# Kernel tuning notes

Hardware: AMD Instinct MI355X
Metric: run time of the kernel (lower is better)

The kernel has to match this reference:

```python
import jax, jax.numpy as jnp
import numpy as np

NEG = -1e9  # stands in for -inf; sparsemax thresholding makes these entries exactly 0


def sparsemax(z):
    """Sparsemax along the last axis (Martins & Astudillo 2016)."""
    K = z.shape[-1]
    z_sorted = -jnp.sort(-z, axis=-1)                      # descending
    kk = jnp.arange(1, K + 1, dtype=z.dtype)
    z_cum = jnp.cumsum(z_sorted, axis=-1)
    support = 1.0 + kk * z_sorted > z_cum                  # [..., K] bool
    k_sup = jnp.sum(support, axis=-1, keepdims=True).astype(z.dtype)
    z_sum = jnp.sum(jnp.where(support, z_sorted, 0.0), axis=-1, keepdims=True)
    tau = (z_sum - 1.0) / k_sup
    return jnp.maximum(z - tau, 0.0)


def setup_inputs() -> dict:
    key = jax.random.key(0)
    ks = jax.random.split(key, 7)
    b, t, e, h = 8, 1024, 128, 8
    x = jax.random.normal(ks[0], (b, t, e), dtype=jnp.float32)
    mask = jax.random.randint(ks[1], (b, t, t), 0, 2, dtype=jnp.int32)
    w_q = jax.random.normal(ks[2], (e, h * e), dtype=jnp.float32) * 0.05
    w_k = jax.random.normal(ks[3], (e, h * e), dtype=jnp.float32) * 0.05
    w_v = jax.random.normal(ks[4], (e, h * e), dtype=jnp.float32) * 0.05
    w_s = jax.random.normal(ks[5], (h, e), dtype=jnp.float32) * 0.05
    b_s = jnp.zeros((h,), dtype=jnp.float32)
    return {"x": x, "mask": mask, "w_q": w_q, "w_k": w_k, "w_v": w_v,
            "w_s": w_s, "b_s": b_s}


def reference(x, mask, w_q, w_k, w_v, w_s, b_s):
    b, t, e = x.shape
    h = w_s.shape[0]
    scale = 1.0 / jnp.sqrt(jnp.asarray(e, x.dtype))  # temperature = emb_dim**0.5

    # projections: each head gets FULL emb_dim width (per original module)
    q = (x @ w_q).reshape(b, t, h, e).transpose(2, 0, 1, 3)  # [h,b,t,e]
    k = (x @ w_k).reshape(b, t, h, e).transpose(2, 0, 1, 3)
    v = (x @ w_v).reshape(b, t, h, e).transpose(2, 0, 1, 3)

    attn = jnp.einsum('hbqe,hbke->hbqk', q * scale, k)       # [h,b,t,t]

    m = mask.astype(bool)[None]                              # [1,b,t,t], broadcast over heads
    inf_mask = jnp.all(m, axis=-1, keepdims=True)            # rows fully masked
    attn = jnp.where(m, NEG, attn)
    attn = jnp.where(inf_mask, 0.0, attn)
    attn = sparsemax(attn)
    attn = jnp.where(inf_mask, 0.0, attn)                    # dropout is identity (p=0)

    out = jnp.einsum('hbqk,hbke->hbqe', attn, v)             # [h,b,t,e]
    out = out.transpose(1, 2, 0, 3)                          # [b,t,h,e]

    sel = jax.nn.softmax(jnp.mean(x, axis=1) @ w_s.T + b_s, axis=-1)  # [b,h]
    return jnp.einsum('bh,bthe->bte', sel, out)              # gated head mix
```

## Files before the change

kernel.cpp:

```cpp
#include <hip/hip_runtime.h>
#include <hip/hip_bf16.h>
#include <math.h>

#define SCALE 0.08838834764831845f

using short8  = __attribute__((ext_vector_type(8))) short;
using short4v = __attribute__((ext_vector_type(4))) short;
using us4     = __attribute__((ext_vector_type(4))) unsigned short;
using f32x4   = __attribute__((ext_vector_type(4))) float;
typedef unsigned long long u64;
typedef unsigned short ushort_t;

static __device__ __forceinline__ ushort_t bf16_of(float f) {
    __hip_bfloat16 h = __float2bfloat16(f);
    return *reinterpret_cast<ushort_t*>(&h);
}
static __device__ __forceinline__ float f_of_bf16(unsigned int u) {
    union { unsigned int i; float f; } v; v.i = u << 16; return v.f;
}

__global__ __launch_bounds__(256)
void prep_all(const float* __restrict__ x, ushort_t* __restrict__ xb,
              const float* __restrict__ wq, const float* __restrict__ wk,
              const float* __restrict__ wv, ushort_t* __restrict__ Wt,
              const int* __restrict__ mask, u64* __restrict__ mp) {
    __shared__ float tile[64][129];
    const int bx = blockIdx.x;
    const int tid = threadIdx.x;
    if (bx < 1024) {
        const int i = bx * 256 + tid;
        float4 v = reinterpret_cast<const float4*>(x)[i];
        short4v o;
        o.x = (short)bf16_of(v.x); o.y = (short)bf16_of(v.y);
        o.z = (short)bf16_of(v.z); o.w = (short)bf16_of(v.w);
        reinterpret_cast<short4v*>(xb)[i] = o;
    } else if (bx < 1072) {
        const int wb = bx - 1024;
        const int mat = wb >> 4;
        const int n0 = (wb & 15) * 64;
        const float* W = (mat == 0) ? wq : (mat == 1) ? wk : wv;
        for (int idx = tid; idx < 8192; idx += 256) {
            const int k = idx >> 6, c = idx & 63;
            tile[c][k] = W[(size_t)k * 1024 + n0 + c];
        }
        __syncthreads();
        for (int idx = tid; idx < 8192; idx += 256) {
            const int c = idx >> 7, k = idx & 127;
            Wt[(size_t)(mat * 1024 + n0 + c) * 128 + k] = bf16_of(tile[c][k]);
        }
    } else {
        const int mb = bx - 1072;
        const int row = mb * 4 + (tid >> 6);
        const int l = tid & 63;
        const int* m = mask + (size_t)row * 1024;
        #pragma unroll
        for (int c = 0; c < 16; ++c) {
            u64 bm = __ballot(m[c * 64 + l] != 0);
            if (l == 0) mp[(size_t)row * 16 + c] = bm;
        }
    }
}

__global__ __launch_bounds__(256)
void proj_gemm(const ushort_t* __restrict__ xb, const ushort_t* __restrict__ Wt,
               ushort_t* __restrict__ Q, ushort_t* __restrict__ K,
               ushort_t* __restrict__ V) {
    const int tid = threadIdx.x;
    const int w = tid >> 6, l = tid & 63;
    const int l15 = l & 15, lq = l >> 4;
    const int m0 = blockIdx.x * 64;
    const int nb = blockIdx.y;
    const int mat = nb >> 4;
    const int n0 = (nb & 15) * 64;
    const int b = m0 >> 10;

    short8 af[4][4];
    #pragma unroll
    for (int at = 0; at < 4; ++at) {
        const ushort_t* ar = xb + (size_t)(m0 + at * 16 + l15) * 128 + lq * 8;
        #pragma unroll
        for (int f = 0; f < 4; ++f)
            af[at][f] = *reinterpret_cast<const short8*>(ar + f * 32);
    }
    const int ng = n0 + w * 16 + l15;
    const ushort_t* br = Wt + (size_t)(mat * 1024 + ng) * 128 + lq * 8;
    short8 bf[4];
    #pragma unroll
    for (int f = 0; f < 4; ++f)
        bf[f] = *reinterpret_cast<const short8*>(br + f * 32);
    f32x4 acc[4];
    #pragma unroll
    for (int at = 0; at < 4; ++at) acc[at] = (f32x4){0.f, 0.f, 0.f, 0.f};
    #pragma unroll
    for (int at = 0; at < 4; ++at)
        #pragma unroll
        for (int f = 0; f < 4; ++f)
            acc[at] = __builtin_amdgcn_mfma_f32_16x16x32_bf16(af[at][f], bf[f], acc[at], 0, 0, 0);

    const int h = ng >> 7, e = ng & 127;
    ushort_t* O = (mat == 0) ? Q : (mat == 1) ? K : V;
    const float scl = (mat == 0) ? SCALE : 1.0f;
    const size_t obase = (size_t)(h * 8 + b) * 131072 + e;
    #pragma unroll
    for (int at = 0; at < 4; ++at)
        #pragma unroll
        for (int r = 0; r < 4; ++r) {
            const int t = (m0 & 1023) + at * 16 + lq * 4 + r;
            O[obase + (size_t)t * 128] = bf16_of(acc[at][r] * scl);
        }
}

__global__ __launch_bounds__(1024)
void sel_kernel(const float* __restrict__ x, const float* __restrict__ wsl,
                const float* __restrict__ bsl, float* __restrict__ sel) {
    __shared__ float part[8][128];
    __shared__ float xm[128];
    __shared__ float lg[8];
    const int b = blockIdx.x;
    const int tid = threadIdx.x;
    const int e = tid & 127, tc = tid >> 7;
    float s = 0.f;
    for (int t = 0; t < 128; ++t)
        s += x[((size_t)b * 1024 + tc * 128 + t) * 128 + e];
    part[tc][e] = s;
    __syncthreads();
    if (tid < 128) {
        float tot = 0.f;
        #pragma unroll
        for (int i = 0; i < 8; ++i) tot += part[i][tid];
        xm[tid] = tot * (1.0f / 1024.0f);
    }
    __syncthreads();
    if (tid < 8) {
        float d = 0.f;
        for (int e2 = 0; e2 < 128; ++e2) d += xm[e2] * wsl[tid * 128 + e2];
        lg[tid] = d + bsl[tid];
    }
    __syncthreads();
    if (tid == 0) {
        float mx = lg[0];
        for (int hh = 1; hh < 8; ++hh) mx = fmaxf(mx, lg[hh]);
        float se = 0.f; float ex[8];
        for (int hh = 0; hh < 8; ++hh) { ex[hh] = expf(lg[hh] - mx); se += ex[hh]; }
        for (int hh = 0; hh < 8; ++hh) sel[b * 8 + hh] = ex[hh] / se;
    }
}

__global__ __launch_bounds__(512, 2)
void attn_kernel(const ushort_t* __restrict__ Qb, const ushort_t* __restrict__ Kb,
                 const ushort_t* __restrict__ Vb, const u64* __restrict__ mp,
                 const float* __restrict__ sel, float* __restrict__ out) {
    __shared__ float S[16 * 1024];
    __shared__ int cnt[16];
    unsigned int* list = reinterpret_cast<unsigned int*>(S);

    const int tid = threadIdx.x;
    const int w = tid >> 6, l = tid & 63;
    const int l15 = l & 15, lq = l >> 4;
    const int hb = (int)blockIdx.x >> 6;
    const int qt = (int)blockIdx.x & 63;
    const int h = hb >> 3, b = hb & 7;
    const int t0 = qt * 16;
    const size_t base = (size_t)hb * 131072;

    if (tid < 16) cnt[tid] = 0;

    short8 qa[4];
    {
        const ushort_t* qrp = Qb + base + (size_t)(t0 + l15) * 128 + lq * 8;
        #pragma unroll
        for (int f = 0; f < 4; ++f)
            qa[f] = *reinterpret_cast<const short8*>(qrp + f * 32);
    }

    f32x4 sc[8];
    #pragma unroll
    for (int i = 0; i < 8; ++i) {
        const int kt = w * 8 + i;
        const ushort_t* krow = Kb + base + (size_t)(kt * 16 + l15) * 128 + lq * 8;
        f32x4 acc = {0.f, 0.f, 0.f, 0.f};
        #pragma unroll
        for (int f = 0; f < 4; ++f) {
            short8 kb = *reinterpret_cast<const short8*>(krow + f * 32);
            acc = __builtin_amdgcn_mfma_f32_16x16x32_bf16(qa[f], kb, acc, 0, 0, 0);
        }
        sc[i] = acc;
    }

    const int rowbase = b * 1024 + t0;
    #pragma unroll
    for (int r = 0; r < 4; ++r) {
        const int q = lq * 4 + r;
        const u64* mrow = mp + (size_t)(rowbase + q) * 16 + w * 2;
        const u64 m0 = mrow[0], m1 = mrow[1];
        #pragma unroll
        for (int i = 0; i < 8; ++i) {
            const u64 mword = (i < 4) ? m0 : m1;
            const int bit = (i & 3) * 16 + l15;
            if ((mword >> bit) & 1ULL) sc[i][r] = -1e30f;
        }
    }

    #pragma unroll
    for (int r = 0; r < 4; ++r) {
        const int q = lq * 4 + r;
        #pragma unroll
        for (int i = 0; i < 8; ++i) {
            const int c = (w * 8 + i) * 4 + (l15 >> 2);
            const int cp = c ^ ((c >> 3) & 7) ^ (q & 7);
            S[q * 1024 + cp * 4 + (l15 & 3)] = sc[i][r];
        }
    }
    __syncthreads();

    const int qrow = 2 * w + (l & 1);
    const int lh = l >> 1;
    float z[32];
    #pragma unroll
    for (int j = 0; j < 8; ++j) {
        const int c = lh + 32 * j;
        const int cp = c ^ ((c >> 3) & 7) ^ (qrow & 7);
        float4 v = *reinterpret_cast<const float4*>(&S[qrow * 1024 + cp * 4]);
        z[4 * j + 0] = v.x; z[4 * j + 1] = v.y;
        z[4 * j + 2] = v.z; z[4 * j + 3] = v.w;
    }
    __syncthreads();

    float s0 = 0.f, c0 = 0.f;
    #pragma unroll
    for (int k = 0; k < 32; ++k) {
        const float zz = z[k];
        if (zz > -1e29f) { s0 += zz; c0 += 1.f; }
    }
    #pragma unroll
    for (int mm = 2; mm < 64; mm <<= 1) {
        s0 += __shfl_xor(s0, mm);
        c0 += __shfl_xor(c0, mm);
    }
    float tau = (c0 > 0.f) ? (s0 - 1.f) / c0 : 3e38f;
    float prev = c0;
    for (int it = 0; it < 64; ++it) {
        float s2 = 0.f, c2 = 0.f;
        #pragma unroll
        for (int k = 0; k < 32; ++k) {
            const float zz = z[k];
            if (zz > tau) { s2 += zz; c2 += 1.f; }
        }
        #pragma unroll
        for (int mm = 2; mm < 64; mm <<= 1) {
            s2 += __shfl_xor(s2, mm);
            c2 += __shfl_xor(c2, mm);
        }
        const int stable = (c2 == prev) ? 1 : 0;
        if (__all(stable)) break;
        if (!stable) { tau = (s2 - 1.f) / c2; prev = c2; }
    }

    #pragma unroll
    for (int j = 0; j < 32; ++j) {
        const float p = z[j] - tau;
        if (p > 0.f) {
            const int k = 4 * lh + 128 * (j >> 2) + (j & 3);
            const int pos = atomicAdd(&cnt[qrow], 1);
            list[qrow * 1024 + pos] = (unsigned int)k | ((unsigned int)bf16_of(p) << 16);
        }
    }
    __syncthreads();

    const int row = tid >> 5;
    const int eq = tid & 31;
    const int n = cnt[row];
    const ushort_t* Vrow = Vb + base;
    const unsigned int* lrow = list + row * 1024;
    float a0 = 0.f, a1 = 0.f, a2 = 0.f, a3 = 0.f;
    for (int j = 0; j < n; ++j) {
        const unsigned int ent = lrow[j];
        const int k = (int)(ent & 0xFFFFu);
        const float p = f_of_bf16(ent >> 16);
        us4 vv = *reinterpret_cast<const us4*>(Vrow + (size_t)k * 128 + eq * 4);
        a0 += p * f_of_bf16(vv.x);
        a1 += p * f_of_bf16(vv.y);
        a2 += p * f_of_bf16(vv.z);
        a3 += p * f_of_bf16(vv.w);
    }
    const float gsel = sel[b * 8 + h];
    float* orow = out + ((size_t)(b * 1024 + t0 + row)) * 128 + eq * 4;
    atomicAdd(&orow[0], gsel * a0);
    atomicAdd(&orow[1], gsel * a1);
    atomicAdd(&orow[2], gsel * a2);
    atomicAdd(&orow[3], gsel * a3);
}

extern "C" void kernel_launch(void* const* d_in, const int* in_sizes, int n_in,
                              void* d_out, int out_size, void* d_ws, size_t ws_size,
                              hipStream_t stream) {
    (void)in_sizes; (void)n_in; (void)ws_size;
    const float* x   = (const float*)d_in[0];
    const int* mask  = (const int*)d_in[1];
    const float* wq  = (const float*)d_in[2];
    const float* wk  = (const float*)d_in[3];
    const float* wv  = (const float*)d_in[4];
    const float* wsl = (const float*)d_in[5];
    const float* bsl = (const float*)d_in[6];
    float* out = (float*)d_out;

    char* wsc = (char*)d_ws;
    float*    sel = (float*)wsc;
    u64*      mp  = (u64*)(wsc + 4096);
    ushort_t* xb  = (ushort_t*)(wsc + 4096 + 1048576);
    ushort_t* Wt  = (ushort_t*)(wsc + 4096 + 1048576 + 2097152);
    ushort_t* Qb  = (ushort_t*)(wsc + 4096 + 1048576 + 2097152 + 786432);
    ushort_t* Kb  = Qb + (size_t)8388608;
    ushort_t* Vb  = Kb + (size_t)8388608;

    hipMemsetAsync(d_out, 0, (size_t)out_size * sizeof(float), stream);
    prep_all<<<3120, 256, 0, stream>>>(x, xb, wq, wk, wv, Wt, mask, mp);
    sel_kernel<<<8, 1024, 0, stream>>>(x, wsl, bsl, sel);
    proj_gemm<<<dim3(128, 48), 256, 0, stream>>>(xb, Wt, Qb, Kb, Vb);
    attn_kernel<<<4096, 512, 0, stream>>>(Qb, Kb, Vb, mp, sel, out);
}
```

Before: 303.9 us.

## Halve attention LDS footprint with two-pass scoring and faster sparsemax threshold search

Scores are now computed in two passes of 512 keys, each staged through a 16x512 LDS buffer, which halves shared memory per block. The launch bound now asks for 8 waves per EU to raise occupancy. Each query row is now owned by one half-wave, so reductions only cross 32 lanes and the barrier before the V accumulation is dropped. The sparsemax threshold iteration now starts from rowmax-1 instead of the mean over unmasked entries, which should need fewer iterations. The tighter register budget may cause spills. The per-row support list is capped at 512 entries, which would give wrong results if a row's support ever exceeded that.

```diff
diff --git a/kernel.cpp b/kernel.cpp
--- a/kernel.cpp
+++ b/kernel.cpp
@@ -146,22 +146,25 @@
     }
 }
 
-__global__ __launch_bounds__(512, 2)
+__global__ __launch_bounds__(512, 8)
 void attn_kernel(const ushort_t* __restrict__ Qb, const ushort_t* __restrict__ Kb,
                  const ushort_t* __restrict__ Vb, const u64* __restrict__ mp,
                  const float* __restrict__ sel, float* __restrict__ out) {
-    __shared__ float S[16 * 1024];
+    __shared__ float S[16 * 512];
     __shared__ int cnt[16];
     unsigned int* list = reinterpret_cast<unsigned int*>(S);
 
     const int tid = threadIdx.x;
     const int w = tid >> 6, l = tid & 63;
     const int l15 = l & 15, lq = l >> 4;
+    const int qrow = tid >> 5;
+    const int lh = l & 31;
     const int hb = (int)blockIdx.x >> 6;
     const int qt = (int)blockIdx.x & 63;
     const int h = hb >> 3, b = hb & 7;
     const int t0 = qt * 16;
     const size_t base = (size_t)hb * 131072;
+    const int rowbase = b * 1024 + t0;
 
     if (tid < 16) cnt[tid] = 0;
 
@@ -173,105 +176,106 @@
             qa[f] = *reinterpret_cast<const short8*>(qrp + f * 32);
     }
 
-    f32x4 sc[8];
-    #pragma unroll
-    for (int i = 0; i < 8; ++i) {
-        const int kt = w * 8 + i;
-        const ushort_t* krow = Kb + base + (size_t)(kt * 16 + l15) * 128 + lq * 8;
-        f32x4 acc = {0.f, 0.f, 0.f, 0.f};
-        #pragma unroll
-        for (int f = 0; f < 4; ++f) {
-            short8 kb = *reinterpret_cast<const short8*>(krow + f * 32);
-            acc = __builtin_amdgcn_mfma_f32_16x16x32_bf16(qa[f], kb, acc, 0, 0, 0);
-        }
-        sc[i] = acc;
-    }
-
-    const int rowbase = b * 1024 + t0;
-    #pragma unroll
-    for (int r = 0; r < 4; ++r) {
-        const int q = lq * 4 + r;
-        const u64* mrow = mp + (size_t)(rowbase + q) * 16 + w * 2;
-        const u64 m0 = mrow[0], m1 = mrow[1];
-        #pragma unroll
-        for (int i = 0; i < 8; ++i) {
-            const u64 mword = (i < 4) ? m0 : m1;
-            const int bit = (i & 3) * 16 + l15;
-            if ((mword >> bit) & 1ULL) sc[i][r] = -1e30f;
-        }
-    }
-
-    #pragma unroll
-    for (int r = 0; r < 4; ++r) {
-        const int q = lq * 4 + r;
-        #pragma unroll
-        for (int i = 0; i < 8; ++i) {
-            const int c = (w * 8 + i) * 4 + (l15 >> 2);
-            const int cp = c ^ ((c >> 3) & 7) ^ (q & 7);
-            S[q * 1024 + cp * 4 + (l15 & 3)] = sc[i][r];
-        }
-    }
-    __syncthreads();
-
-    const int qrow = 2 * w + (l & 1);
-    const int lh = l >> 1;
     float z[32];
-    #pragma unroll
-    for (int j = 0; j < 8; ++j) {
-        const int c = lh + 32 * j;
-        const int cp = c ^ ((c >> 3) & 7) ^ (qrow & 7);
-        float4 v = *reinterpret_cast<const float4*>(&S[qrow * 1024 + cp * 4]);
-        z[4 * j + 0] = v.x; z[4 * j + 1] = v.y;
-        z[4 * j + 2] = v.z; z[4 * j + 3] = v.w;
-    }
-    __syncthreads();
-
-    float s0 = 0.f, c0 = 0.f;
-    #pragma unroll
-    for (int k = 0; k < 32; ++k) {
-        const float zz = z[k];
-        if (zz > -1e29f) { s0 += zz; c0 += 1.f; }
-    }
-    #pragma unroll
-    for (int mm = 2; mm < 64; mm <<= 1) {
-        s0 += __shfl_xor(s0, mm);
-        c0 += __shfl_xor(c0, mm);
-    }
-    float tau = (c0 > 0.f) ? (s0 - 1.f) / c0 : 3e38f;
-    float prev = c0;
-    for (int it = 0; it < 64; ++it) {
-        float s2 = 0.f, c2 = 0.f;
-        #pragma unroll
-        for (int k = 0; k < 32; ++k) {
-            const float zz = z[k];
-            if (zz > tau) { s2 += zz; c2 += 1.f; }
-        }
-        #pragma unroll
-        for (int mm = 2; mm < 64; mm <<= 1) {
-            s2 += __shfl_xor(s2, mm);
-            c2 += __shfl_xor(c2, mm);
-        }
-        const int stable = (c2 == prev) ? 1 : 0;
-        if (__all(stable)) break;
-        if (!stable) { tau = (s2 - 1.f) / c2; prev = c2; }
-    }
-
-    #pragma unroll
-    for (int j = 0; j < 32; ++j) {
-        const float p = z[j] - tau;
+
+    #pragma unroll
+    for (int pass = 0; pass < 2; ++pass) {
+        f32x4 sc[4];
+        #pragma unroll
+        for (int i = 0; i < 4; ++i) {
+            const int kt = pass * 32 + w * 4 + i;
+            const ushort_t* krow = Kb + base + (size_t)(kt * 16 + l15) * 128 + lq * 8;
+            f32x4 acc = {0.f, 0.f, 0.f, 0.f};
+            #pragma unroll
+            for (int f = 0; f < 4; ++f) {
+                short8 kb = *reinterpret_cast<const short8*>(krow + f * 32);
+                acc = __builtin_amdgcn_mfma_f32_16x16x32_bf16(qa[f], kb, acc, 0, 0, 0);
+            }
+            sc[i] = acc;
+        }
+        #pragma unroll
+        for (int r = 0; r < 4; ++r) {
+            const int q = lq * 4 + r;
+            const u64 mw = mp[(size_t)(rowbase + q) * 16 + pass * 8 + w];
+            #pragma unroll
+            for (int i = 0; i < 4; ++i) {
+                const int bit = i * 16 + l15;
+                if ((mw >> bit) & 1ULL) sc[i][r] = -1e30f;
+            }
+        }
+        #pragma unroll
+        for (int r = 0; r < 4; ++r) {
+            const int q = lq * 4 + r;
+            #pragma unroll
+            for (int i = 0; i < 4; ++i) {
+                const int c = (w * 4 + i) * 4 + (l15 >> 2);
+                const int cp = c ^ ((c >> 3) & 7) ^ (q & 7);
+                S[q * 512 + cp * 4 + (l15 & 3)] = sc[i][r];
+            }
+        }
+        __syncthreads();
+        #pragma unroll
+        for (int j = 0; j < 4; ++j) {
+            const int c = lh + 32 * j;
+            const int cp = c ^ ((c >> 3) & 7) ^ (qrow & 7);
+            float4 v = *reinterpret_cast<const float4*>(&S[qrow * 512 + cp * 4]);
+            z[pass * 16 + 4 * j + 0] = v.x; z[pass * 16 + 4 * j + 1] = v.y;
+            z[pass * 16 + 4 * j + 2] = v.z; z[pass * 16 + 4 * j + 3] = v.w;
+        }
+        __syncthreads();
+    }
+
+    float m16[16];
+    #pragma unroll
+    for (int j = 0; j < 16; ++j) m16[j] = fmaxf(z[j], z[j + 16]);
+    #pragma unroll
+    for (int j = 0; j < 8; ++j) m16[j] = fmaxf(m16[j], m16[j + 8]);
+    #pragma unroll
+    for (int j = 0; j < 4; ++j) m16[j] = fmaxf(m16[j], m16[j + 4]);
+    float mx = fmaxf(fmaxf(m16[0], m16[1]), fmaxf(m16[2], m16[3]));
+    #pragma unroll
+    for (int mm = 1; mm <= 16; mm <<= 1) mx = fmaxf(mx, __shfl_xor(mx, mm));
+
+    float tau;
+    if (mx < -1e29f) {
+        tau = 3e38f;
+    } else {
+        tau = mx - 1.0f;
+        unsigned prev = 0xFFFFFFFFu;
+        for (int it = 0; it < 64; ++it) {
+            float s2 = 0.f; unsigned c2 = 0u;
+            #pragma unroll
+            for (int k = 0; k < 32; ++k) {
+                const float zz = z[k];
+                s2 += (zz > tau) ? zz : 0.f;
+                c2 += (zz > tau) ? 1u : 0u;
+            }
+            #pragma unroll
+            for (int mm = 1; mm <= 16; mm <<= 1) {
+                s2 += __shfl_xor(s2, mm);
+                c2 += __shfl_xor(c2, mm);
+            }
+            if (c2 == prev) break;
+            tau = (s2 - 1.f) / (float)c2;
+            prev = c2;
+        }
+    }
+
+    #pragma unroll
+    for (int jj = 0; jj < 32; ++jj) {
+        const float p = z[jj] - tau;
         if (p > 0.f) {
-            const int k = 4 * lh + 128 * (j >> 2) + (j & 3);
+            const int k = ((jj & 16) << 5) + 4 * lh + 128 * ((jj >> 2) & 3) + (jj & 3);
             const int pos = atomicAdd(&cnt[qrow], 1);
-            list[qrow * 1024 + pos] = (unsigned int)k | ((unsigned int)bf16_of(p) << 16);
-        }
-    }
-    __syncthreads();
-
-    const int row = tid >> 5;
+            if (pos < 512)
+                list[qrow * 512 + pos] = (unsigned int)k | ((unsigned int)bf16_of(p) << 16);
+        }
+    }
+
     const int eq = tid & 31;
-    const int n = cnt[row];
+    int n = cnt[qrow]; n = (n < 512) ? n : 512;
     const ushort_t* Vrow = Vb + base;
-    const unsigned int* lrow = list + row * 1024;
+    const unsigned int* lrow = list + qrow * 512;
     float a0 = 0.f, a1 = 0.f, a2 = 0.f, a3 = 0.f;
     for (int j = 0; j < n; ++j) {
         const unsigned int ent = lrow[j];
@@ -284,7 +288,7 @@
         a3 += p * f_of_bf16(vv.w);
     }
     const float gsel = sel[b * 8 + h];
-    float* orow = out + ((size_t)(b * 1024 + t0 + row)) * 128 + eq * 4;
+    float* orow = out + ((size_t)(b * 1024 + t0 + qrow)) * 128 + eq * 4;
     atomicAdd(&orow[0], gsel * a0);
     atomicAdd(&orow[1], gsel * a1);
     atomicAdd(&orow[2], gsel * a2);
```

Result: slower. 351.0 us (+15.5%).
